# Optimization experiments

Hardware: AMD Instinct MI355X
Metric: run time of the kernel (lower is better)

Reference implementation:

```python
import jax, jax.numpy as jnp
import numpy as np
import math

N_EXP = 64
TOP_K = 2
EVAL_CAPACITY = 1.25
MIN_CAPACITY = 4


def _capacity(num_tokens):
    cap = math.floor(TOP_K * EVAL_CAPACITY * num_tokens / N_EXP)
    cap += cap % 2
    return max(cap, MIN_CAPACITY)


def setup_inputs() -> dict:
    key = jax.random.key(0)
    k1, k2 = jax.random.split(key)
    x = jax.random.normal(k1, (4096, 2048), dtype=jnp.float32)
    w_g = jax.random.normal(k2, (64, 2048), dtype=jnp.float32) * 0.02
    return {"x": x, "w_g": w_g}


def reference(x, w_g):
    # x: [T, D], w_g: [E, D]
    T, D = x.shape
    cap = _capacity(T)

    logits = x @ w_g.T                                   # [T, E]
    top_v, top_i = jax.lax.top_k(logits, TOP_K)          # [T, K]

    # softmax over only the top-k logits (others -> -inf)
    rows = jnp.arange(T)[:, None]
    masked = jnp.full_like(logits, -jnp.inf).at[rows, top_i].set(top_v)
    router_probs = jax.nn.softmax(masked, axis=-1)       # [T, E]

    # Capacity-aware assignment: flatten (token, k) pairs in row-major order,
    # exactly matching the original sequential double loop. The slot for each
    # attempt is the exclusive prefix count of attempts to that expert; once an
    # expert's count exceeds capacity, all later attempts are rejected, which
    # matches the sequential semantics (usage only stops growing at capacity).
    flat_e = top_i.reshape(-1)                           # [T*K]
    tok = jnp.repeat(jnp.arange(T), TOP_K)               # [T*K]
    onehot = jax.nn.one_hot(flat_e, N_EXP, dtype=jnp.int32)   # [T*K, E]
    cum = jnp.cumsum(onehot, axis=0)                     # inclusive counts
    slot = cum[jnp.arange(T * TOP_K), flat_e] - 1        # exclusive prefix count
    assigned = slot < cap

    used_capacity = jnp.minimum(cum[-1], cap).astype(jnp.int32)   # [E]

    # Route rejected attempts to a scratch slot `cap`, then slice it off.
    safe_slot = jnp.where(assigned, slot, cap)
    w = router_probs[tok, flat_e]                        # [T*K]

    cb_weight = (jnp.zeros((T, N_EXP, cap + 1), dtype=x.dtype)
                 .at[tok, flat_e, safe_slot].set(w))[..., :cap]
    sec_mask = (jnp.zeros((T, N_EXP, cap + 1), dtype=bool)
                .at[tok, flat_e, safe_slot].set(True))[..., :cap]

    return used_capacity, cb_weight, sec_mask
```

## Files before the change

kernel.cpp:

```cpp
#include <hip/hip_runtime.h>
#include <math.h>

#define T_TOK 4096
#define D_DIM 2048
#define NEXP  64
#define CAP   160

#define TPB   4
#define NGB   (T_TOK / TPB)
#define NZB   2048

typedef float vfloat4 __attribute__((ext_vector_type(4)));

__global__ __launch_bounds__(256) void fused_main(
    const float* __restrict__ x, const float* __restrict__ wg,
    float* __restrict__ out, int out_size,
    int* __restrict__ topi, float* __restrict__ topw)
{
    const int bid = blockIdx.x;
    const int tid = threadIdx.x;

    if (bid >= NGB) {
        const int zb = bid - NGB;
        const size_t n4 = (size_t)out_size >> 2;
        vfloat4* o4 = (vfloat4*)out;
        const vfloat4 z = {0.f, 0.f, 0.f, 0.f};
        const size_t stride = (size_t)NZB * 256;
        for (size_t i = (size_t)zb * 256 + tid; i < n4; i += stride)
            __builtin_nontemporal_store(z, &o4[i]);
        if (zb == 0 && tid == 0) {
            for (size_t i = n4 << 2; i < (size_t)out_size; ++i) out[i] = 0.f;
        }
        return;
    }

    const int e    = tid & 63;
    const int w    = __builtin_amdgcn_readfirstlane(tid >> 6);
    const int tok0 = bid * TPB;
    const int wk0  = w * (D_DIM / 4);

    float acc[TPB] = {0.f, 0.f, 0.f, 0.f};

    const float* __restrict__ wrow = wg + (size_t)e * D_DIM + wk0;

    for (int c = 0; c < (D_DIM / 4) / 32; ++c) {
        vfloat4 b[8];
#pragma unroll
        for (int j = 0; j < 8; ++j)
            b[j] = *(const vfloat4*)(wrow + c * 32 + j * 4);
#pragma unroll
        for (int t = 0; t < TPB; ++t) {
            const float* __restrict__ xp =
                x + (size_t)(tok0 + t) * D_DIM + wk0 + c * 32;
            float s = 0.f;
#pragma unroll
            for (int j = 0; j < 8; ++j) {
                s += xp[j*4+0] * b[j].x + xp[j*4+1] * b[j].y
                   + xp[j*4+2] * b[j].z + xp[j*4+3] * b[j].w;
            }
            acc[t] += s;
        }
    }

    __shared__ float sAcc[4][TPB][NEXP];
#pragma unroll
    for (int t = 0; t < TPB; ++t)
        sAcc[w][t][e] = acc[t];
    __syncthreads();

    const int t = w;
    float v = sAcc[0][t][e] + sAcc[1][t][e] + sAcc[2][t][e] + sAcc[3][t][e];

    float v1 = v;         int i1 = e;
    float v2 = -INFINITY; int i2 = NEXP;
#pragma unroll
    for (int off = 32; off >= 1; off >>= 1) {
        const float ov1 = __shfl_xor(v1, off, 64);
        const int   oi1 = __shfl_xor(i1, off, 64);
        const float ov2 = __shfl_xor(v2, off, 64);
        const int   oi2 = __shfl_xor(i2, off, 64);
        const bool firstMine = (v1 > ov1) || (v1 == ov1 && i1 < oi1);
        const float n1  = firstMine ? v1  : ov1;
        const int   ni1 = firstMine ? i1  : oi1;
        const float c1  = firstMine ? ov1 : v1;
        const int   ci1 = firstMine ? oi1 : i1;
        const float c2  = firstMine ? v2  : ov2;
        const int   ci2 = firstMine ? i2  : oi2;
        const bool secondC1 = (c1 > c2) || (c1 == c2 && ci1 < ci2);
        v1 = n1;                      i1 = ni1;
        v2 = secondC1 ? c1 : c2;      i2 = secondC1 ? ci1 : ci2;
    }

    if (e == 0) {
        const int gt = tok0 + t;
        const float r  = expf(v2 - v1);
        const float s1 = 1.0f / (1.0f + r);
        topi[2 * gt + 0] = i1;
        topi[2 * gt + 1] = i2;
        topw[2 * gt + 0] = s1;
        topw[2 * gt + 1] = r * s1;
    }
}

__global__ __launch_bounds__(64) void scatter_assign(
    const int* __restrict__ topi, const float* __restrict__ topw,
    float* __restrict__ out)
{
    __shared__ int cnt[NEXP];
    const int lane = threadIdx.x;
    cnt[lane] = 0;
    __syncthreads();

    float* __restrict__ cb   = out + NEXP;
    float* __restrict__ mask = out + NEXP + (size_t)T_TOK * NEXP * CAP;

    const unsigned long long lt = ((unsigned long long)1 << lane) - 1ull;
    const int NCH = (T_TOK * 2) / 64;

    int   e  = topi[lane];
    float tw = topw[lane];

    for (int c = 0; c < NCH; ++c) {
        int   en  = 0;
        float twn = 0.f;
        if (c + 1 < NCH) {
            en  = topi[(c + 1) * 64 + lane];
            twn = topw[(c + 1) * 64 + lane];
        }

        unsigned long long m = ~0ull;
#pragma unroll
        for (int b = 0; b < 6; ++b) {
            const unsigned long long vb = __ballot((e >> b) & 1);
            m &= ((e >> b) & 1) ? vb : ~vb;
        }
        const int p     = __popcll(m & lt);
        const int base  = cnt[e];
        const int slot  = base + p;
        if (p == 0) cnt[e] = base + __popcll(m);

        if (slot < CAP) {
            const int f = c * 64 + lane;
            const int t = f >> 1;
            const size_t off = ((size_t)t * NEXP + e) * CAP + slot;
            cb[off]   = tw;
            mask[off] = 1.0f;
        }
        e = en; tw = twn;
    }

    int used = cnt[lane];
    if (used > CAP) used = CAP;
    out[lane] = (float)used;
}

extern "C" void kernel_launch(void* const* d_in, const int* in_sizes, int n_in,
                              void* d_out, int out_size, void* d_ws, size_t ws_size,
                              hipStream_t stream)
{
    const float* x  = (const float*)d_in[0];
    const float* wg = (const float*)d_in[1];
    float* out = (float*)d_out;

    int*   topi = (int*)d_ws;
    float* topw = (float*)(topi + T_TOK * 2);

    fused_main<<<NGB + NZB, 256, 0, stream>>>(x, wg, out, out_size, topi, topw);
    scatter_assign<<<1, 64, 0, stream>>>(topi, topw, out);
}
```

Before: 459.9 us.

## Co-schedule zeroing waves with GEMV and parallelize capacity scatter per expert

The main kernel becomes 512-thread blocks in which wave 0 computes full-depth router logits for four tokens, so the shared-memory split-K reduction is gone, while the other seven waves zero the output with nontemporal stores. The single-wave sequential scatter is replaced by 64 blocks, one per expert, each building per-lane match bitmasks and using a prefix scan to assign slots in order. This is meant to remove the serial 128-iteration scatter bottleneck and to overlap zeroing with the logit compute. In exchange, each compute wave loops over the full 2048 depth alone, and the scalar tail zeroing for sizes not divisible by four is dropped.

```diff
diff --git a/kernel.cpp b/kernel.cpp
--- a/kernel.cpp
+++ b/kernel.cpp
@@ -6,152 +6,154 @@
 #define NEXP  64
 #define CAP   160
 
-#define TPB   4
-#define NGB   (T_TOK / TPB)
-#define NZB   2048
+#define NGB   1024
 
 typedef float vfloat4 __attribute__((ext_vector_type(4)));
 
-__global__ __launch_bounds__(256) void fused_main(
+__global__ __launch_bounds__(512) void fused_main(
     const float* __restrict__ x, const float* __restrict__ wg,
     float* __restrict__ out, int out_size,
     int* __restrict__ topi, float* __restrict__ topw)
 {
-    const int bid = blockIdx.x;
-    const int tid = threadIdx.x;
+    const int tid  = threadIdx.x;
+    const int w    = __builtin_amdgcn_readfirstlane(tid >> 6);
+    const int lane = tid & 63;
+    const int bid  = blockIdx.x;
 
-    if (bid >= NGB) {
-        const int zb = bid - NGB;
+    if (w != 0) {
+        const int fw = bid * 7 + (w - 1);
         const size_t n4 = (size_t)out_size >> 2;
         vfloat4* o4 = (vfloat4*)out;
         const vfloat4 z = {0.f, 0.f, 0.f, 0.f};
-        const size_t stride = (size_t)NZB * 256;
-        for (size_t i = (size_t)zb * 256 + tid; i < n4; i += stride)
+        const size_t stride = (size_t)7 * NGB * 64;
+        for (size_t i = (size_t)fw * 64 + lane; i < n4; i += stride)
             __builtin_nontemporal_store(z, &o4[i]);
-        if (zb == 0 && tid == 0) {
-            for (size_t i = n4 << 2; i < (size_t)out_size; ++i) out[i] = 0.f;
-        }
         return;
     }
 
-    const int e    = tid & 63;
-    const int w    = __builtin_amdgcn_readfirstlane(tid >> 6);
-    const int tok0 = bid * TPB;
-    const int wk0  = w * (D_DIM / 4);
+    const int e    = lane;
+    const int tok0 = bid * 4;
+    float acc[4] = {0.f, 0.f, 0.f, 0.f};
 
-    float acc[TPB] = {0.f, 0.f, 0.f, 0.f};
+    const vfloat4* __restrict__ wrow = (const vfloat4*)(wg + (size_t)e * D_DIM);
 
-    const float* __restrict__ wrow = wg + (size_t)e * D_DIM + wk0;
-
-    for (int c = 0; c < (D_DIM / 4) / 32; ++c) {
+    for (int c = 0; c < D_DIM / 32; ++c) {
         vfloat4 b[8];
 #pragma unroll
         for (int j = 0; j < 8; ++j)
-            b[j] = *(const vfloat4*)(wrow + c * 32 + j * 4);
+            b[j] = wrow[c * 8 + j];
 #pragma unroll
-        for (int t = 0; t < TPB; ++t) {
-            const float* __restrict__ xp =
-                x + (size_t)(tok0 + t) * D_DIM + wk0 + c * 32;
+        for (int t = 0; t < 4; ++t) {
+            const vfloat4* __restrict__ xv =
+                (const vfloat4*)(x + (size_t)(tok0 + t) * D_DIM) + c * 8;
             float s = 0.f;
 #pragma unroll
             for (int j = 0; j < 8; ++j) {
-                s += xp[j*4+0] * b[j].x + xp[j*4+1] * b[j].y
-                   + xp[j*4+2] * b[j].z + xp[j*4+3] * b[j].w;
+                const vfloat4 xa = xv[j];
+                s += xa.x * b[j].x + xa.y * b[j].y + xa.z * b[j].z + xa.w * b[j].w;
             }
             acc[t] += s;
         }
     }
 
-    __shared__ float sAcc[4][TPB][NEXP];
 #pragma unroll
-    for (int t = 0; t < TPB; ++t)
-        sAcc[w][t][e] = acc[t];
-    __syncthreads();
-
-    const int t = w;
-    float v = sAcc[0][t][e] + sAcc[1][t][e] + sAcc[2][t][e] + sAcc[3][t][e];
-
-    float v1 = v;         int i1 = e;
-    float v2 = -INFINITY; int i2 = NEXP;
+    for (int t = 0; t < 4; ++t) {
+        float v1 = acc[t];    int i1 = e;
+        float v2 = -INFINITY; int i2 = NEXP;
 #pragma unroll
-    for (int off = 32; off >= 1; off >>= 1) {
-        const float ov1 = __shfl_xor(v1, off, 64);
-        const int   oi1 = __shfl_xor(i1, off, 64);
-        const float ov2 = __shfl_xor(v2, off, 64);
-        const int   oi2 = __shfl_xor(i2, off, 64);
-        const bool firstMine = (v1 > ov1) || (v1 == ov1 && i1 < oi1);
-        const float n1  = firstMine ? v1  : ov1;
-        const int   ni1 = firstMine ? i1  : oi1;
-        const float c1  = firstMine ? ov1 : v1;
-        const int   ci1 = firstMine ? oi1 : i1;
-        const float c2  = firstMine ? v2  : ov2;
-        const int   ci2 = firstMine ? i2  : oi2;
-        const bool secondC1 = (c1 > c2) || (c1 == c2 && ci1 < ci2);
-        v1 = n1;                      i1 = ni1;
-        v2 = secondC1 ? c1 : c2;      i2 = secondC1 ? ci1 : ci2;
-    }
-
-    if (e == 0) {
-        const int gt = tok0 + t;
-        const float r  = expf(v2 - v1);
-        const float s1 = 1.0f / (1.0f + r);
-        topi[2 * gt + 0] = i1;
-        topi[2 * gt + 1] = i2;
-        topw[2 * gt + 0] = s1;
-        topw[2 * gt + 1] = r * s1;
+        for (int off = 32; off >= 1; off >>= 1) {
+            const float ov1 = __shfl_xor(v1, off, 64);
+            const int   oi1 = __shfl_xor(i1, off, 64);
+            const float ov2 = __shfl_xor(v2, off, 64);
+            const int   oi2 = __shfl_xor(i2, off, 64);
+            const bool firstMine = (v1 > ov1) || (v1 == ov1 && i1 < oi1);
+            const float n1  = firstMine ? v1  : ov1;
+            const int   ni1 = firstMine ? i1  : oi1;
+            const float c1  = firstMine ? ov1 : v1;
+            const int   ci1 = firstMine ? oi1 : i1;
+            const float c2  = firstMine ? v2  : ov2;
+            const int   ci2 = firstMine ? i2  : oi2;
+            const bool secondC1 = (c1 > c2) || (c1 == c2 && ci1 < ci2);
+            v1 = n1;                 i1 = ni1;
+            v2 = secondC1 ? c1 : c2; i2 = secondC1 ? ci1 : ci2;
+        }
+        if (e == 0) {
+            const int gt = tok0 + t;
+            const float r  = expf(v2 - v1);
+            const float s1 = 1.0f / (1.0f + r);
+            topi[2 * gt + 0] = i1;
+            topi[2 * gt + 1] = i2;
+            topw[2 * gt + 0] = s1;
+            topw[2 * gt + 1] = r * s1;
+        }
     }
 }
 
-__global__ __launch_bounds__(64) void scatter_assign(
+__global__ __launch_bounds__(64) void scatter_par(
     const int* __restrict__ topi, const float* __restrict__ topw,
     float* __restrict__ out)
 {
-    __shared__ int cnt[NEXP];
+    const int e    = blockIdx.x;
     const int lane = threadIdx.x;
-    cnt[lane] = 0;
-    __syncthreads();
+
+    const int4* __restrict__ tp = (const int4*)topi + lane * 32;
+
+    unsigned long long m0 = 0ull, m1 = 0ull;
+#pragma unroll
+    for (int i = 0; i < 16; ++i) {
+        const int4 a = tp[i];
+        unsigned long long bits =
+              (unsigned long long)(a.x == e)
+            | ((unsigned long long)(a.y == e) << 1)
+            | ((unsigned long long)(a.z == e) << 2)
+            | ((unsigned long long)(a.w == e) << 3);
+        m0 |= bits << (i * 4);
+    }
+#pragma unroll
+    for (int i = 16; i < 32; ++i) {
+        const int4 a = tp[i];
+        unsigned long long bits =
+              (unsigned long long)(a.x == e)
+            | ((unsigned long long)(a.y == e) << 1)
+            | ((unsigned long long)(a.z == e) << 2)
+            | ((unsigned long long)(a.w == e) << 3);
+        m1 |= bits << ((i - 16) * 4);
+    }
+
+    const int c = __popcll(m0) + __popcll(m1);
+
+    int v = c;
+#pragma unroll
+    for (int off = 1; off < 64; off <<= 1) {
+        const int n = __shfl_up(v, off, 64);
+        if (lane >= off) v += n;
+    }
+    int running = v - c;
+    const int total = __shfl(v, 63, 64);
 
     float* __restrict__ cb   = out + NEXP;
     float* __restrict__ mask = out + NEXP + (size_t)T_TOK * NEXP * CAP;
 
-    const unsigned long long lt = ((unsigned long long)1 << lane) - 1ull;
-    const int NCH = (T_TOK * 2) / 64;
-
-    int   e  = topi[lane];
-    float tw = topw[lane];
-
-    for (int c = 0; c < NCH; ++c) {
-        int   en  = 0;
-        float twn = 0.f;
-        if (c + 1 < NCH) {
-            en  = topi[(c + 1) * 64 + lane];
-            twn = topw[(c + 1) * 64 + lane];
+    const int fbase = lane * 128;
+    unsigned long long mm = m0;
+#pragma unroll
+    for (int half = 0; half < 2; ++half) {
+        while (mm) {
+            const int b = __builtin_ctzll(mm);
+            mm &= mm - 1;
+            const int f = fbase + half * 64 + b;
+            const int slot = running++;
+            if (slot < CAP) {
+                const size_t off = ((size_t)(f >> 1) * NEXP + e) * CAP + slot;
+                cb[off]   = topw[f];
+                mask[off] = 1.0f;
+            }
         }
-
-        unsigned long long m = ~0ull;
-#pragma unroll
-        for (int b = 0; b < 6; ++b) {
-            const unsigned long long vb = __ballot((e >> b) & 1);
-            m &= ((e >> b) & 1) ? vb : ~vb;
-        }
-        const int p     = __popcll(m & lt);
-        const int base  = cnt[e];
-        const int slot  = base + p;
-        if (p == 0) cnt[e] = base + __popcll(m);
-
-        if (slot < CAP) {
-            const int f = c * 64 + lane;
-            const int t = f >> 1;
-            const size_t off = ((size_t)t * NEXP + e) * CAP + slot;
-            cb[off]   = tw;
-            mask[off] = 1.0f;
-        }
-        e = en; tw = twn;
+        mm = m1;
     }
 
-    int used = cnt[lane];
-    if (used > CAP) used = CAP;
-    out[lane] = (float)used;
+    if (lane == 0)
+        out[e] = (float)(total < CAP ? total : CAP);
 }
 
 extern "C" void kernel_launch(void* const* d_in, const int* in_sizes, int n_in,
@@ -165,6 +167,6 @@
     int*   topi = (int*)d_ws;
     float* topw = (float*)(topi + T_TOK * 2);
 
-    fused_main<<<NGB + NZB, 256, 0, stream>>>(x, wg, out, out_size, topi, topw);
-    scatter_assign<<<1, 64, 0, stream>>>(topi, topw, out);
+    fused_main<<<NGB, 512, 0, stream>>>(x, wg, out, out_size, topi, topw);
+    scatter_par<<<64, 64, 0, stream>>>(topi, topw, out);
 }
```

After: 463.6 us. Within noise of the previous version (+0.8%).
